# Performance work log

Measured on AMD Instinct MI355X. Metric: run time of the kernel, lower is better.

## Reference

```python
import jax, jax.numpy as jnp
import numpy as np

B, S, D = 2, 1024, 2048
H, KV, HD = 16, 4, 128
GROUPS = H // KV
THETA = 10000.0


def act_quant(xr, xi):
    # per-token 8-bit absmax quantization over last dim, joint scale for re/im, STE
    amax = jnp.maximum(jnp.max(jnp.abs(xr), -1, keepdims=True),
                       jnp.max(jnp.abs(xi), -1, keepdims=True))
    s = 127.0 / jnp.maximum(amax, 1e-5)
    qr = jnp.clip(jnp.round(xr * s), -128, 127) / s
    qi = jnp.clip(jnp.round(xi * s), -128, 127) / s
    return xr + jax.lax.stop_gradient(qr - xr), xi + jax.lax.stop_gradient(qi - xi)


def weight_quant(wr, wi):
    # Fairy+-i direction quantization: each weight -> scale * d, d in {+1,-1,+i,-i}; STE
    mag = jnp.mean(jnp.sqrt(wr * wr + wi * wi))
    use_re = jnp.abs(wr) >= jnp.abs(wi)
    qr = jnp.where(use_re, jnp.sign(wr) * mag, 0.0)
    qi = jnp.where(use_re, 0.0, jnp.sign(wi) * mag)
    return wr + jax.lax.stop_gradient(qr - wr), wi + jax.lax.stop_gradient(qi - wi)


def complex_linear(xr, xi, wr, wi):
    xr, xi = act_quant(xr, xi)
    wr, wi = weight_quant(wr, wi)
    o_re = xr @ wr - xi @ wi
    o_im = xr @ wi + xi @ wr
    return o_re, o_im


def rotate_half(x):
    h = x.shape[-1] // 2
    return jnp.concatenate([-x[..., h:], x[..., :h]], axis=-1)


def rope_tables():
    inv_freq = 1.0 / (THETA ** (jnp.arange(0, HD, 2, dtype=jnp.float32) / HD))
    pos = jnp.arange(S, dtype=jnp.float32)
    freqs = pos[:, None] * inv_freq[None, :]          # [S, HD/2]
    emb = jnp.concatenate([freqs, freqs], axis=-1)    # [S, HD]
    return jnp.cos(emb)[None, None], jnp.sin(emb)[None, None]  # [1,1,S,HD]


def _heads(x, n):
    # [B,S,n*HD] -> [B,n,S,HD]
    return x.reshape(B, S, n, HD).transpose(0, 2, 1, 3)


def _attn(hidden_real, hidden_imag, wq_re, wq_im, wk_re, wk_im,
          wv_re, wv_im, wo_re, wo_im):
    q_re, q_im = complex_linear(hidden_real, hidden_imag, wq_re, wq_im)
    k_re, k_im = complex_linear(hidden_real, hidden_imag, wk_re, wk_im)
    v_re, v_im = complex_linear(hidden_real, hidden_imag, wv_re, wv_im)

    q_re, q_im = _heads(q_re, H), _heads(q_im, H)      # [B,H,S,HD]
    k_re, k_im = _heads(k_re, KV), _heads(k_im, KV)    # [B,KV,S,HD]
    v_re, v_im = _heads(v_re, KV), _heads(v_im, KV)

    cos, sin = rope_tables()
    # RoPE applied only to real components of q and k
    q_re = q_re * cos + rotate_half(q_re) * sin
    k_re = k_re * cos + rotate_half(k_re) * sin

    # GQA repeat
    k_re = jnp.repeat(k_re, GROUPS, axis=1)
    k_im = jnp.repeat(k_im, GROUPS, axis=1)
    v_re = jnp.repeat(v_re, GROUPS, axis=1)
    v_im = jnp.repeat(v_im, GROUPS, axis=1)

    # real scores = Re(q . conj(k)) = q_re.k_re + q_im.k_im
    scores = (jnp.einsum('bhqd,bhkd->bhqk', q_re, k_re) +
              jnp.einsum('bhqd,bhkd->bhqk', q_im, k_im)) / jnp.sqrt(jnp.float32(HD))
    causal = jnp.tril(jnp.ones((S, S), dtype=bool))
    scores = jnp.where(causal[None, None], scores, jnp.finfo(scores.dtype).min)
    attn = jax.nn.softmax(scores, axis=-1)

    o_re = jnp.einsum('bhqk,bhkd->bhqd', attn, v_re)
    o_im = jnp.einsum('bhqk,bhkd->bhqd', attn, v_im)
    o_re = o_re.transpose(0, 2, 1, 3).reshape(B, S, H * HD)
    o_im = o_im.transpose(0, 2, 1, 3).reshape(B, S, H * HD)

    out_re, out_im = complex_linear(o_re, o_im, wo_re, wo_im)
    return jnp.stack([out_re, out_im])  # [2,B,S,D]


def setup_inputs() -> dict:
    key = jax.random.key(0)
    ks = jax.random.split(key, 12)
    w = lambda k, shp: jax.random.normal(k, shp, dtype=jnp.float32) * 0.02
    return {
        'hidden_real': jax.random.normal(ks[0], (B, S, D), dtype=jnp.float32),
        'hidden_imag': jax.random.normal(ks[1], (B, S, D), dtype=jnp.float32),
        'wq_re': w(ks[2], (D, H * HD)), 'wq_im': w(ks[3], (D, H * HD)),
        'wk_re': w(ks[4], (D, KV * HD)), 'wk_im': w(ks[5], (D, KV * HD)),
        'wv_re': w(ks[6], (D, KV * HD)), 'wv_im': w(ks[7], (D, KV * HD)),
        'wo_re': w(ks[8], (H * HD, D)), 'wo_im': w(ks[9], (H * HD, D)),
    }


def reference(hidden_real, hidden_imag, wq_re, wq_im, wk_re, wk_im,
              wv_re, wv_im, wo_re, wo_im):
    return _attn(hidden_real, hidden_imag, wq_re, wq_im, wk_re, wk_im,
                 wv_re, wv_im, wo_re, wo_im)
```

## Files before the change

### kernel.cpp

```cpp
#include <hip/hip_runtime.h>
#include <stdint.h>

#define B_   2
#define S_   1024
#define D_   2048
#define H_   16
#define KV_  4
#define HD_  128
#define NTOK (B_ * S_)
#define QD   (H_ * HD_)
#define KD   (KV_ * HD_)

using i32x4  = __attribute__((ext_vector_type(4)))  int;
using i32x16 = __attribute__((ext_vector_type(16))) int;
using f32x4  = __attribute__((ext_vector_type(4)))  float;
using bf16x8 = __attribute__((ext_vector_type(8)))  short;

#define LN1E4_OVER_64 0.14391156831212725f

__device__ __forceinline__ float bf2f(uint16_t u) { return __uint_as_float((uint32_t)u << 16); }
__device__ __forceinline__ uint16_t f2bf(float f) {
    uint32_t u = __float_as_uint(f);
    return (uint16_t)((u + 0x7FFFu + ((u >> 16) & 1u)) >> 16);
}

__device__ __forceinline__ i32x4 neg_i8x16(i32x4 x) {
    i32x4 r;
#pragma unroll
    for (int i = 0; i < 4; ++i) {
        uint32_t nx = ~(uint32_t)x[i];
        r[i] = (int)(((nx & 0x7F7F7F7Fu) + 0x01010101u) ^ (nx & 0x80808080u));
    }
    return r;
}

__global__ __launch_bounds__(256)
void act_quant_i8_kernel(const float* __restrict__ xr, const float* __restrict__ xi,
                         int8_t* __restrict__ qr, int8_t* __restrict__ qi,
                         float* __restrict__ invs)
{
    const int tok = blockIdx.x, t = threadIdx.x;
    const float* pr = xr + (size_t)tok * 2048 + t * 8;
    const float* pi = xi + (size_t)tok * 2048 + t * 8;
    float4 r0 = *(const float4*)pr, r1 = *(const float4*)(pr + 4);
    float4 i0 = *(const float4*)pi, i1 = *(const float4*)(pi + 4);
    float am = fmaxf(fmaxf(fmaxf(fabsf(r0.x), fabsf(r0.y)), fmaxf(fabsf(r0.z), fabsf(r0.w))),
                     fmaxf(fmaxf(fabsf(r1.x), fabsf(r1.y)), fmaxf(fabsf(r1.z), fabsf(r1.w))));
    am = fmaxf(am, fmaxf(fmaxf(fmaxf(fabsf(i0.x), fabsf(i0.y)), fmaxf(fabsf(i0.z), fabsf(i0.w))),
                         fmaxf(fmaxf(fabsf(i1.x), fabsf(i1.y)), fmaxf(fabsf(i1.z), fabsf(i1.w)))));
    __shared__ float red[256];
    red[t] = am;
    __syncthreads();
    for (int st = 128; st > 0; st >>= 1) {
        if (t < st) red[t] = fmaxf(red[t], red[t + st]);
        __syncthreads();
    }
    const float s = 127.0f / fmaxf(red[0], 1e-5f);
    if (t == 0) invs[tok] = 1.0f / s;
#define Q8(x) ((uint32_t)(uint8_t)(int8_t)(int)fminf(fmaxf(rintf((x) * s), -128.f), 127.f))
    uint32_t a0 = Q8(r0.x) | (Q8(r0.y) << 8) | (Q8(r0.z) << 16) | (Q8(r0.w) << 24);
    uint32_t a1 = Q8(r1.x) | (Q8(r1.y) << 8) | (Q8(r1.z) << 16) | (Q8(r1.w) << 24);
    uint32_t b0 = Q8(i0.x) | (Q8(i0.y) << 8) | (Q8(i0.z) << 16) | (Q8(i0.w) << 24);
    uint32_t b1 = Q8(i1.x) | (Q8(i1.y) << 8) | (Q8(i1.z) << 16) | (Q8(i1.w) << 24);
#undef Q8
    *(uint32_t*)(qr + (size_t)tok * 2048 + t * 8)     = a0;
    *(uint32_t*)(qr + (size_t)tok * 2048 + t * 8 + 4) = a1;
    *(uint32_t*)(qi + (size_t)tok * 2048 + t * 8)     = b0;
    *(uint32_t*)(qi + (size_t)tok * 2048 + t * 8 + 4) = b1;
}

__global__ __launch_bounds__(256)
void decode_kernel(const float* __restrict__ wr, const float* __restrict__ wi,
                   int N, int8_t* __restrict__ psr, int8_t* __restrict__ psi,
                   int n_off, float* __restrict__ mag_out)
{
    __shared__ alignas(16) int8_t tr[2][64][80];
    __shared__ float red[256];
    const int n0 = blockIdx.x * 64, k0 = blockIdx.y * 64;
    float msum = 0.f;
    for (int idx = threadIdx.x; idx < 4096; idx += 256) {
        int j = idx & 63, i = idx >> 6;
        size_t g = (size_t)(k0 + i) * N + n0 + j;
        float a = wr[g], b = wi[g];
        msum += sqrtf(a * a + b * b);
        int8_t sr, si;
        if (fabsf(a) >= fabsf(b)) {
            sr = (a > 0.f) ? 1 : ((a < 0.f) ? -1 : 0);
            si = 0;
        } else {
            sr = 0;
            si = (b > 0.f) ? 1 : ((b < 0.f) ? -1 : 0);
        }
        tr[0][j][i] = sr;
        tr[1][j][i] = si;
    }
    red[threadIdx.x] = msum;
    __syncthreads();
    for (int st = 128; st > 0; st >>= 1) {
        if (threadIdx.x < st) red[threadIdx.x] += red[threadIdx.x + st];
        __syncthreads();
    }
    if (threadIdx.x == 0) atomicAdd(mag_out, red[0]);
    int8_t* planes[2] = { psr, psi };
    for (int idx = threadIdx.x; idx < 512; idx += 256) {
        int p = idx >> 8, rem = idx & 255, n = rem >> 2, c = rem & 3;
        int4 v = *(const int4*)&tr[p][n][c * 16];
        *(int4*)(planes[p] + (size_t)(n_off + n0 + n) * 2048 + k0 + c * 16) = v;
    }
}

__device__ __forceinline__ void async_copy16(const void* g, void* l) {
    __builtin_amdgcn_global_load_lds((const __attribute__((address_space(1))) void*)g,
                                     (__attribute__((address_space(3))) void*)l, 16, 0, 0);
}

template <int MODE>
__global__ __launch_bounds__(256, 3)
void gemm_i8_kernel(const int8_t* __restrict__ axr, const int8_t* __restrict__ axi,
                    const int8_t* __restrict__ bsr, const int8_t* __restrict__ bsi,
                    int Nout, const float* __restrict__ invs,
                    const float* __restrict__ mag_sums,
                    float magc0, float magc1, float magc2,
                    float* o_re, float* o_im,
                    uint16_t* kbr, uint16_t* kbi, uint16_t* vbr, uint16_t* vbi)
{
    __shared__ alignas(16) int8_t smem[2][24576];
    const int tid = threadIdx.x;
    const int wav = tid >> 6, lane = tid & 63;
    const int tileM = blockIdx.y * 64, tileN = blockIdx.x * 128;
    const int K = 2048;

    i32x16 pre[2] = {};
    i32x16 pim[2] = {};

    auto issue_tile = [&](int k0, int buf) {
#pragma unroll
        for (int i = 0; i < 6; ++i) {
            int q = wav + 4 * i;
            const int8_t* g;
            int8_t* l;
            if (q < 8) {
                int pl = q >> 2, c = q & 3;
                g = (pl ? axi : axr) + (size_t)(tileM + lane) * K + k0 + c * 16;
                l = &smem[buf][pl * 4096 + (c * 64 + lane) * 16];
            } else {
                int r = q - 8;
                int pl = r >> 3, s = r & 7, c = s >> 1, m0 = (s & 1) << 6;
                g = (pl ? bsi : bsr) + (size_t)(tileN + m0 + lane) * K + k0 + c * 16;
                l = &smem[buf][8192 + pl * 8192 + (c * 128 + m0 + lane) * 16];
            }
            async_copy16(g, l);
        }
    };

    issue_tile(0, 0);
    issue_tile(64, 1);

    for (int k = 0; k < 32; ++k) {
        if (k == 31) { asm volatile("s_waitcnt vmcnt(0)" ::: "memory"); }
        else         { asm volatile("s_waitcnt vmcnt(6)" ::: "memory"); }
        asm volatile("s_barrier" ::: "memory");
        const int8_t* sb = smem[k & 1];
#pragma unroll
        for (int s = 0; s < 2; ++s) {
            const int cc = 2 * s + (lane >> 5);
            const int rA = lane & 31;
            const int rB = wav * 32 + (lane & 31);
            i32x4 fxr[2], fxi[2];
#pragma unroll
            for (int mb = 0; mb < 2; ++mb) {
                int off = (cc * 64 + rA + mb * 32) * 16;
                fxr[mb] = *(const i32x4*)&sb[off];
                fxi[mb] = *(const i32x4*)&sb[4096 + off];
            }
            i32x4 fbr, fbi;
            {
                int off = (cc * 128 + rB) * 16;
                fbr = *(const i32x4*)&sb[8192 + off];
                fbi = *(const i32x4*)&sb[16384 + off];
            }
            const i32x4 fbin = neg_i8x16(fbi);
#pragma unroll
            for (int mb = 0; mb < 2; ++mb) {
                pre[mb] = __builtin_amdgcn_mfma_i32_32x32x32_i8(fxr[mb], fbr,  pre[mb], 0, 0, 0);
                pre[mb] = __builtin_amdgcn_mfma_i32_32x32x32_i8(fxi[mb], fbin, pre[mb], 0, 0, 0);
                pim[mb] = __builtin_amdgcn_mfma_i32_32x32x32_i8(fxr[mb], fbi,  pim[mb], 0, 0, 0);
                pim[mb] = __builtin_amdgcn_mfma_i32_32x32x32_i8(fxi[mb], fbr,  pim[mb], 0, 0, 0);
            }
        }
        asm volatile("s_barrier" ::: "memory");
        if (k + 2 < 32) issue_tile((k + 2) * 64, k & 1);
    }

    const int ln31 = lane & 31, lq = lane >> 5;
    const int gn = tileN + wav * 32 + ln31;
    float mag;
    if (MODE == 0)
        mag = (gn < 2048) ? mag_sums[0] * magc0
            : (gn < 2560) ? mag_sums[1] * magc1
                          : mag_sums[2] * magc2;
    else
        mag = mag_sums[0] * magc0;
#pragma unroll
    for (int mb = 0; mb < 2; ++mb) {
#pragma unroll
        for (int r = 0; r < 16; ++r) {
            const int row = (r & 3) + 8 * (r >> 2) + 4 * lq;
            const int gm = tileM + mb * 32 + row;
            const float sc = mag * invs[gm];
            const float re = (float)pre[mb][r] * sc;
            const float im = (float)pim[mb][r] * sc;
            if (MODE == 1) {
                o_re[(size_t)gm * Nout + gn] = re;
                o_im[(size_t)gm * Nout + gn] = im;
            } else {
                const int s = gm & (S_ - 1), bb = gm >> 10;
                if (gn < 2048) {
                    o_re[(size_t)gm * 2048 + gn] = re;
                    o_im[(size_t)gm * 2048 + gn] = im;
                } else if (gn < 2560) {
                    int c = gn - 2048, kvh = c >> 7, d = c & 127;
                    size_t off = ((size_t)(bb * KV_ + kvh) * S_ + s) * 128 + d;
                    kbr[off] = f2bf(re);
                    kbi[off] = f2bf(im);
                } else {
                    int c = gn - 2560, kvh = c >> 7, d = c & 127;
                    size_t off = ((size_t)(bb * KV_ + kvh) * S_ + s) * 128 + d;
                    vbr[off] = f2bf(re);
                    vbi[off] = f2bf(im);
                }
            }
        }
    }
}

__global__ __launch_bounds__(256)
void rope_q_kernel(const float* __restrict__ q_re, const float* __restrict__ q_im,
                   uint16_t* __restrict__ qb_re, uint16_t* __restrict__ qb_im)
{
    int gidx = blockIdx.x * 256 + threadIdx.x;
    int j = gidx & 15, h = (gidx >> 4) & 15, tok = gidx >> 8;
    int s = tok & (S_ - 1), b = tok >> 10;
    int d0 = j * 4;
    size_t ib = (size_t)tok * 2048 + h * 128;
    float4 r0 = *(const float4*)&q_re[ib + d0];
    float4 r1 = *(const float4*)&q_re[ib + d0 + 64];
    float4 i0 = *(const float4*)&q_im[ib + d0];
    float4 i1 = *(const float4*)&q_im[ib + d0 + 64];
    float ro0[4], ro1[4];
    float rv0[4] = { r0.x, r0.y, r0.z, r0.w };
    float rv1[4] = { r1.x, r1.y, r1.z, r1.w };
#pragma unroll
    for (int t = 0; t < 4; ++t) {
        float f = __expf(-(float)(d0 + t) * LN1E4_OVER_64);
        float sn, c;
        __sincosf((float)s * f, &sn, &c);
        ro0[t] = rv0[t] * c - rv1[t] * sn;
        ro1[t] = rv1[t] * c + rv0[t] * sn;
    }
    size_t ob = ((size_t)(b * H_ + h) * S_ + s) * 128;
    ushort4 w;
    w = (ushort4){ f2bf(ro0[0]), f2bf(ro0[1]), f2bf(ro0[2]), f2bf(ro0[3]) };
    *(ushort4*)&qb_re[ob + d0] = w;
    w = (ushort4){ f2bf(ro1[0]), f2bf(ro1[1]), f2bf(ro1[2]), f2bf(ro1[3]) };
    *(ushort4*)&qb_re[ob + d0 + 64] = w;
    w = (ushort4){ f2bf(i0.x), f2bf(i0.y), f2bf(i0.z), f2bf(i0.w) };
    *(ushort4*)&qb_im[ob + d0] = w;
    w = (ushort4){ f2bf(i1.x), f2bf(i1.y), f2bf(i1.z), f2bf(i1.w) };
    *(ushort4*)&qb_im[ob + d0 + 64] = w;
}

__global__ __launch_bounds__(256)
void rope_k_kernel(uint16_t* __restrict__ kb_re)
{
    int gidx = blockIdx.x * 256 + threadIdx.x;
    int j = gidx & 15, kvh = (gidx >> 4) & 3;
    int rest = gidx >> 6;
    int s = rest & (S_ - 1), b = rest >> 10;
    int d0 = j * 4;
    size_t base = ((size_t)(b * KV_ + kvh) * S_ + s) * 128;
    ushort4 u0 = *(const ushort4*)&kb_re[base + d0];
    ushort4 u1 = *(const ushort4*)&kb_re[base + d0 + 64];
    float rv0[4] = { bf2f(u0.x), bf2f(u0.y), bf2f(u0.z), bf2f(u0.w) };
    float rv1[4] = { bf2f(u1.x), bf2f(u1.y), bf2f(u1.z), bf2f(u1.w) };
    float ro0[4], ro1[4];
#pragma unroll
    for (int t = 0; t < 4; ++t) {
        float f = __expf(-(float)(d0 + t) * LN1E4_OVER_64);
        float sn, c;
        __sincosf((float)s * f, &sn, &c);
        ro0[t] = rv0[t] * c - rv1[t] * sn;
        ro1[t] = rv1[t] * c + rv0[t] * sn;
    }
    *(ushort4*)&kb_re[base + d0]      = (ushort4){ f2bf(ro0[0]), f2bf(ro0[1]), f2bf(ro0[2]), f2bf(ro0[3]) };
    *(ushort4*)&kb_re[base + d0 + 64] = (ushort4){ f2bf(ro1[0]), f2bf(ro1[1]), f2bf(ro1[2]), f2bf(ro1[3]) };
}

__global__ __launch_bounds__(256)
void vtrans_kernel(const uint16_t* __restrict__ vbr, const uint16_t* __restrict__ vbi,
                   uint16_t* __restrict__ vtr, uint16_t* __restrict__ vti)
{
    __shared__ uint16_t t[32][36];
    const int pl = blockIdx.z & 1, bk = blockIdx.z >> 1;
    const int s0 = blockIdx.x * 32, d0 = blockIdx.y * 32;
    const uint16_t* src = (pl ? vbi : vbr) + ((size_t)bk * S_) * 128;
    uint16_t*       dst = (pl ? vti : vtr) + ((size_t)bk * 128) * S_;
    const int r = threadIdx.x >> 3, c = (threadIdx.x & 7) * 4;
    *(ushort4*)&t[r][c] = *(const ushort4*)&src[(size_t)(s0 + r) * 128 + d0 + c];
    __syncthreads();
    ushort4 o = (ushort4){ t[c][r], t[c + 1][r], t[c + 2][r], t[c + 3][r] };
    *(ushort4*)&dst[(size_t)(d0 + r) * S_ + s0 + c] = o;
}

__global__ __launch_bounds__(256)
void attn_mfma_kernel(const uint16_t* __restrict__ qb_re, const uint16_t* __restrict__ qb_im,
                      const uint16_t* __restrict__ kb_re, const uint16_t* __restrict__ kb_im,
                      const uint16_t* __restrict__ vt_re, const uint16_t* __restrict__ vt_im,
                      float* __restrict__ o_re, float* __restrict__ o_im)
{
    __shared__ alignas(16) uint16_t sbuf[2][16384];
    __shared__ alignas(16) uint16_t sp[4][16][40];

    const int tid = threadIdx.x;
    const int w = tid >> 6, lane = tid & 63;
    const int r16 = lane & 15, q4 = lane >> 4;
    const int h = blockIdx.y, b = blockIdx.z;
    const int qt = b ? blockIdx.x : (gridDim.x - 1 - blockIdx.x);
    const int kvh = h >> 2;
    const int q0 = qt * 64, qw0 = q0 + w * 16;

    bf16x8 qfr[4], qfi[4];
    {
        const size_t qbase = ((size_t)(b * H_ + h) * S_ + qw0 + r16) * 128;
#pragma unroll
        for (int ks = 0; ks < 4; ++ks) {
            const int col = ks * 32 + q4 * 8;
            qfr[ks] = *(const bf16x8*)&qb_re[qbase + col];
            qfi[ks] = *(const bf16x8*)&qb_im[qbase + col];
        }
    }

    f32x4 oa[2][8] = {};
    float m_r[4] = { -3e38f, -3e38f, -3e38f, -3e38f };
    float l_r[4] = { 0.f, 0.f, 0.f, 0.f };

    const size_t kgbase0 = (size_t)(b * KV_ + kvh) * S_ * 128;
    const uint16_t* vre = vt_re + (size_t)(b * KV_ + kvh) * 128 * (size_t)S_;
    const uint16_t* vim = vt_im + (size_t)(b * KV_ + kvh) * 128 * (size_t)S_;

    const uint16_t* kp[4];
    const uint16_t* vp[4];
#pragma unroll
    for (int i = 0; i < 4; ++i) {
        const int kch = (i & 1) * 8 + w * 2 + (lane >> 5);
        kp[i] = ((i >> 1) ? kb_im : kb_re) + kgbase0 + (size_t)(lane & 31) * 128 + kch * 8;
        const int vch = (i & 1) * 2 + (w >> 1);
        const int vd  = ((w & 1) << 6) | lane;
        vp[i] = ((i >> 1) ? vim : vre) + (size_t)vd * S_ + vch * 8;
    }

    auto issue_tile = [&](int kt, int buf) {
#pragma unroll
        for (int i = 0; i < 4; ++i)
            async_copy16(kp[i] + (size_t)kt * 4096, &sbuf[buf][w * 512 + i * 2048]);
#pragma unroll
        for (int i = 0; i < 4; ++i)
            async_copy16(vp[i] + (size_t)kt * 32, &sbuf[buf][8192 + w * 512 + i * 2048]);
    };

    const int nk = (q0 + 64) >> 5;

    issue_tile(0, 0);
    issue_tile(1, 1);

    for (int k = 0; k < nk; ++k) {
        if (k == nk - 1) { asm volatile("s_waitcnt vmcnt(0)" ::: "memory"); }
        else             { asm volatile("s_waitcnt vmcnt(8)" ::: "memory"); }
        asm volatile("s_barrier" ::: "memory");
        const uint16_t* sb = sbuf[k & 1];
        const int c0 = k << 5;

        if (c0 <= qw0 + 15) {
            f32x4 sc[2] = {};
#pragma unroll
            for (int cblk = 0; cblk < 2; ++cblk) {
                const int krow = cblk * 16 + r16;
#pragma unroll
                for (int ks = 0; ks < 4; ++ks) {
                    const int koff = (ks * 4 + q4) * 256 + krow * 8;
                    bf16x8 kr = *(const bf16x8*)&sb[koff];
                    bf16x8 ki = *(const bf16x8*)&sb[4096 + koff];
                    sc[cblk] = __builtin_amdgcn_mfma_f32_16x16x32_bf16(qfr[ks], kr, sc[cblk], 0, 0, 0);
                    sc[cblk] = __builtin_amdgcn_mfma_f32_16x16x32_bf16(qfi[ks], ki, sc[cblk], 0, 0, 0);
                }
            }
#pragma unroll
            for (int cblk = 0; cblk < 2; ++cblk)
#pragma unroll
                for (int reg = 0; reg < 4; ++reg) {
                    float sval = sc[cblk][reg] * 0.08838834764831845f;
                    const int rowg = qw0 + q4 * 4 + reg;
                    const int colg = c0 + cblk * 16 + r16;
                    if (colg > rowg) sval = -3e38f;
                    sc[cblk][reg] = sval;
                }
            float al[4];
#pragma unroll
            for (int reg = 0; reg < 4; ++reg) {
                float mx = fmaxf(sc[0][reg], sc[1][reg]);
#pragma unroll
                for (int msk = 1; msk < 16; msk <<= 1) mx = fmaxf(mx, __shfl_xor(mx, msk));
                const float mn = fmaxf(m_r[reg], mx);
                al[reg] = __expf(m_r[reg] - mn);
                const float p0 = __expf(sc[0][reg] - mn);
                const float p1 = __expf(sc[1][reg] - mn);
                sc[0][reg] = p0; sc[1][reg] = p1;
                float rs = p0 + p1;
#pragma unroll
                for (int msk = 1; msk < 16; msk <<= 1) rs += __shfl_xor(rs, msk);
                l_r[reg] = l_r[reg] * al[reg] + rs;
                m_r[reg] = mn;
            }
#pragma unroll
            for (int cblk = 0; cblk < 2; ++cblk)
#pragma unroll
                for (int reg = 0; reg < 4; ++reg)
                    sp[w][q4 * 4 + reg][cblk * 16 + r16] = f2bf(sc[cblk][reg]);
#pragma unroll
            for (int dblk = 0; dblk < 8; ++dblk)
#pragma unroll
                for (int reg = 0; reg < 4; ++reg) {
                    oa[0][dblk][reg] *= al[reg];
                    oa[1][dblk][reg] *= al[reg];
                }
            bf16x8 pf = *(const bf16x8*)&sp[w][r16][q4 * 8];
#pragma unroll
            for (int dblk = 0; dblk < 8; ++dblk) {
                const int voff = 8192 + q4 * 1024 + (dblk * 16 + r16) * 8;
                bf16x8 vr = *(const bf16x8*)&sb[voff];
                bf16x8 vi = *(const bf16x8*)&sb[4096 + voff];
                oa[0][dblk] = __builtin_amdgcn_mfma_f32_16x16x32_bf16(pf, vr, oa[0][dblk], 0, 0, 0);
                oa[1][dblk] = __builtin_amdgcn_mfma_f32_16x16x32_bf16(pf, vi, oa[1][dblk], 0, 0, 0);
            }
        }

        asm volatile("s_barrier" ::: "memory");
        if (k + 2 < nk) issue_tile(k + 2, k & 1);
    }

    float inv[4];
#pragma unroll
    for (int reg = 0; reg < 4; ++reg) inv[reg] = 1.f / l_r[reg];
#pragma unroll
    for (int dblk = 0; dblk < 8; ++dblk) {
        const int col = h * 128 + dblk * 16 + r16;
#pragma unroll
        for (int reg = 0; reg < 4; ++reg) {
            const size_t tok = (size_t)b * S_ + qw0 + q4 * 4 + reg;
            o_re[tok * 2048 + col] = oa[0][dblk][reg] * inv[reg];
            o_im[tok * 2048 + col] = oa[1][dblk][reg] * inv[reg];
        }
    }
}

extern "C" void kernel_launch(void* const* d_in, const int* in_sizes, int n_in,
                              void* d_out, int out_size, void* d_ws, size_t ws_size,
                              hipStream_t stream)
{
    const float* hr    = (const float*)d_in[0];
    const float* hi    = (const float*)d_in[1];
    const float* wq_re = (const float*)d_in[2];
    const float* wq_im = (const float*)d_in[3];
    const float* wk_re = (const float*)d_in[4];
    const float* wk_im = (const float*)d_in[5];
    const float* wv_re = (const float*)d_in[6];
    const float* wv_im = (const float*)d_in[7];
    const float* wo_re = (const float*)d_in[8];
    const float* wo_im = (const float*)d_in[9];
    float* out = (float*)d_out;
    char*  base = (char*)d_ws;

    const size_t MB4  = (size_t)2048 * 2048;
    const size_t QKVP = (size_t)3072 * 2048;
    const size_t KVE  = (size_t)B_ * KV_ * S_ * 128;

    float*   mags   = (float*)(base);
    float*   invs1  = (float*)(base + 1024);
    float*   invs2  = (float*)(base + 9216);
    int8_t*  xr_q   = (int8_t*)(base + 32768);
    int8_t*  xi_q   = xr_q + MB4;
    int8_t*  qkv_sr = xi_q + MB4;
    int8_t*  qkv_si = qkv_sr + QKVP;
    int8_t*  qkv_ns = qkv_si + QKVP;
    int8_t*  wo_sr  = qkv_ns + QKVP;
    int8_t*  wo_si  = wo_sr + MB4;
    int8_t*  wo_ns  = wo_si + MB4;
    float*   q_re   = (float*)(wo_ns + MB4);
    float*   q_im   = q_re + MB4;
    uint16_t* kb_re = (uint16_t*)(q_im + MB4);
    uint16_t* kb_im = kb_re + KVE;
    uint16_t* vb_re = kb_im + KVE;
    uint16_t* vb_im = vb_re + KVE;
    uint16_t* vt_re = (uint16_t*)xr_q;
    uint16_t* vt_im = (uint16_t*)xi_q;
    uint16_t* qb_re = (uint16_t*)qkv_sr;
    uint16_t* qb_im = (uint16_t*)(qkv_sr + 8388608);

    hipMemsetAsync(mags, 0, 16, stream);

    decode_kernel<<<dim3(32, 32), 256, 0, stream>>>(wq_re, wq_im, 2048, qkv_sr, qkv_si, 0,    mags + 0);
    decode_kernel<<<dim3(8, 32),  256, 0, stream>>>(wk_re, wk_im, 512,  qkv_sr, qkv_si, 2048, mags + 1);
    decode_kernel<<<dim3(8, 32),  256, 0, stream>>>(wv_re, wv_im, 512,  qkv_sr, qkv_si, 2560, mags + 2);
    decode_kernel<<<dim3(32, 32), 256, 0, stream>>>(wo_re, wo_im, 2048, wo_sr, wo_si, 0,      mags + 3);

    act_quant_i8_kernel<<<NTOK, 256, 0, stream>>>(hr, hi, xr_q, xi_q, invs1);

    gemm_i8_kernel<0><<<dim3(24, 32), 256, 0, stream>>>(
        xr_q, xi_q, qkv_sr, qkv_si, 0, invs1, mags,
        1.0f / (float)((size_t)D_ * QD), 1.0f / (float)((size_t)D_ * KD), 1.0f / (float)((size_t)D_ * KD),
        q_re, q_im, kb_re, kb_im, vb_re, vb_im);

    rope_q_kernel<<<NTOK * H_ * 16 / 256, 256, 0, stream>>>(q_re, q_im, qb_re, qb_im);
    rope_k_kernel<<<NTOK * KV_ * 16 / 256, 256, 0, stream>>>(kb_re);
    vtrans_kernel<<<dim3(S_ / 32, 128 / 32, B_ * KV_ * 2), 256, 0, stream>>>(vb_re, vb_im, vt_re, vt_im);

    attn_mfma_kernel<<<dim3(S_ / 64, H_, B_), 256, 0, stream>>>(
        qb_re, qb_im, kb_re, kb_im, vt_re, vt_im, q_re, q_im);

    act_quant_i8_kernel<<<NTOK, 256, 0, stream>>>(q_re, q_im, xr_q, xi_q, invs2);

    gemm_i8_kernel<1><<<dim3(16, 32), 256, 0, stream>>>(
        xr_q, xi_q, wo_sr, wo_si, 2048, invs2, mags + 3,
        1.0f / (float)((size_t)QD * D_), 0.f, 0.f,
        out, out + MB4, nullptr, nullptr, nullptr, nullptr);
}
```

Before: 464.2 us.

## Fuse RoPE into QKV GEMM epilogue and emit bf16 attention output

The QKV GEMM epilogue now applies RoPE directly, using an LDS exchange to fetch the rotate-half partner column, and writes bf16 Q and K in head-major layout. This removes the separate rope_q and rope_k kernels and the fp32 Q round trip through global memory. The attention kernel now writes bf16 output, and a new bf16-input activation quantizer reads it, halving that traffic. The cost is an extra LDS pass and barriers in the GEMM epilogue, plus bf16 rounding of the attention output before quantization, which could slightly change the quantized values.

```diff
diff --git a/kernel.cpp b/kernel.cpp
--- a/kernel.cpp
+++ b/kernel.cpp
@@ -62,6 +62,48 @@
     uint32_t a1 = Q8(r1.x) | (Q8(r1.y) << 8) | (Q8(r1.z) << 16) | (Q8(r1.w) << 24);
     uint32_t b0 = Q8(i0.x) | (Q8(i0.y) << 8) | (Q8(i0.z) << 16) | (Q8(i0.w) << 24);
     uint32_t b1 = Q8(i1.x) | (Q8(i1.y) << 8) | (Q8(i1.z) << 16) | (Q8(i1.w) << 24);
+#undef Q8
+    *(uint32_t*)(qr + (size_t)tok * 2048 + t * 8)     = a0;
+    *(uint32_t*)(qr + (size_t)tok * 2048 + t * 8 + 4) = a1;
+    *(uint32_t*)(qi + (size_t)tok * 2048 + t * 8)     = b0;
+    *(uint32_t*)(qi + (size_t)tok * 2048 + t * 8 + 4) = b1;
+}
+
+__global__ __launch_bounds__(256)
+void act_quant_bf16_kernel(const uint16_t* __restrict__ xr, const uint16_t* __restrict__ xi,
+                           int8_t* __restrict__ qr, int8_t* __restrict__ qi,
+                           float* __restrict__ invs)
+{
+    const int tok = blockIdx.x, t = threadIdx.x;
+    uint4 rv = *(const uint4*)(xr + (size_t)tok * 2048 + t * 8);
+    uint4 iv = *(const uint4*)(xi + (size_t)tok * 2048 + t * 8);
+    float fr[8], fi[8];
+    const uint32_t* ru = (const uint32_t*)&rv;
+    const uint32_t* iu = (const uint32_t*)&iv;
+#pragma unroll
+    for (int i = 0; i < 4; ++i) {
+        fr[2 * i]     = __uint_as_float(ru[i] << 16);
+        fr[2 * i + 1] = __uint_as_float(ru[i] & 0xFFFF0000u);
+        fi[2 * i]     = __uint_as_float(iu[i] << 16);
+        fi[2 * i + 1] = __uint_as_float(iu[i] & 0xFFFF0000u);
+    }
+    float am = 0.f;
+#pragma unroll
+    for (int i = 0; i < 8; ++i) am = fmaxf(am, fmaxf(fabsf(fr[i]), fabsf(fi[i])));
+    __shared__ float red[256];
+    red[t] = am;
+    __syncthreads();
+    for (int st = 128; st > 0; st >>= 1) {
+        if (t < st) red[t] = fmaxf(red[t], red[t + st]);
+        __syncthreads();
+    }
+    const float s = 127.0f / fmaxf(red[0], 1e-5f);
+    if (t == 0) invs[tok] = 1.0f / s;
+#define Q8(x) ((uint32_t)(uint8_t)(int8_t)(int)fminf(fmaxf(rintf((x) * s), -128.f), 127.f))
+    uint32_t a0 = Q8(fr[0]) | (Q8(fr[1]) << 8) | (Q8(fr[2]) << 16) | (Q8(fr[3]) << 24);
+    uint32_t a1 = Q8(fr[4]) | (Q8(fr[5]) << 8) | (Q8(fr[6]) << 16) | (Q8(fr[7]) << 24);
+    uint32_t b0 = Q8(fi[0]) | (Q8(fi[1]) << 8) | (Q8(fi[2]) << 16) | (Q8(fi[3]) << 24);
+    uint32_t b1 = Q8(fi[4]) | (Q8(fi[5]) << 8) | (Q8(fi[6]) << 16) | (Q8(fi[7]) << 24);
 #undef Q8
     *(uint32_t*)(qr + (size_t)tok * 2048 + t * 8)     = a0;
     *(uint32_t*)(qr + (size_t)tok * 2048 + t * 8 + 4) = a1;
@@ -122,6 +164,7 @@
                     const float* __restrict__ mag_sums,
                     float magc0, float magc1, float magc2,
                     float* o_re, float* o_im,
+                    uint16_t* qbr, uint16_t* qbi,
                     uint16_t* kbr, uint16_t* kbi, uint16_t* vbr, uint16_t* vbi)
 {
     __shared__ alignas(16) int8_t smem[2][24576];
@@ -201,99 +244,68 @@
                           : mag_sums[2] * magc2;
     else
         mag = mag_sums[0] * magc0;
-#pragma unroll
-    for (int mb = 0; mb < 2; ++mb) {
-#pragma unroll
-        for (int r = 0; r < 16; ++r) {
-            const int row = (r & 3) + 8 * (r >> 2) + 4 * lq;
-            const int gm = tileM + mb * 32 + row;
-            const float sc = mag * invs[gm];
-            const float re = (float)pre[mb][r] * sc;
-            const float im = (float)pim[mb][r] * sc;
-            if (MODE == 1) {
-                o_re[(size_t)gm * Nout + gn] = re;
-                o_im[(size_t)gm * Nout + gn] = im;
-            } else {
+
+    if (MODE == 0 && tileN < 2560) {
+        float* lds_ex = (float*)smem;
+        const int d = wav * 32 + ln31;
+        __syncthreads();
+#pragma unroll
+        for (int mb = 0; mb < 2; ++mb)
+#pragma unroll
+            for (int r = 0; r < 16; ++r) {
+                const int row = mb * 32 + (r & 3) + 8 * (r >> 2) + 4 * lq;
+                lds_ex[d * 65 + row] = (float)pre[mb][r] * (mag * invs[tileM + row]);
+            }
+        __syncthreads();
+        const float fd = __expf(-(float)(d & 63) * LN1E4_OVER_64);
+#pragma unroll
+        for (int mb = 0; mb < 2; ++mb)
+#pragma unroll
+            for (int r = 0; r < 16; ++r) {
+                const int row = mb * 32 + (r & 3) + 8 * (r >> 2) + 4 * lq;
+                const int gm = tileM + row;
                 const int s = gm & (S_ - 1), bb = gm >> 10;
-                if (gn < 2048) {
-                    o_re[(size_t)gm * 2048 + gn] = re;
-                    o_im[(size_t)gm * 2048 + gn] = im;
-                } else if (gn < 2560) {
-                    int c = gn - 2048, kvh = c >> 7, d = c & 127;
-                    size_t off = ((size_t)(bb * KV_ + kvh) * S_ + s) * 128 + d;
-                    kbr[off] = f2bf(re);
+                const float sc = mag * invs[gm];
+                const float re = (float)pre[mb][r] * sc;
+                const float im = (float)pim[mb][r] * sc;
+                const float prt = lds_ex[(d ^ 64) * 65 + row];
+                float sn, cs;
+                __sincosf((float)s * fd, &sn, &cs);
+                const float ro = (d < 64) ? (re * cs - prt * sn) : (re * cs + prt * sn);
+                if (tileN < 2048) {
+                    const int hh = tileN >> 7;
+                    const size_t off = ((size_t)(bb * H_ + hh) * S_ + s) * 128 + d;
+                    qbr[off] = f2bf(ro);
+                    qbi[off] = f2bf(im);
+                } else {
+                    const int kvh = (tileN - 2048) >> 7;
+                    const size_t off = ((size_t)(bb * KV_ + kvh) * S_ + s) * 128 + d;
+                    kbr[off] = f2bf(ro);
                     kbi[off] = f2bf(im);
+                }
+            }
+    } else {
+#pragma unroll
+        for (int mb = 0; mb < 2; ++mb)
+#pragma unroll
+            for (int r = 0; r < 16; ++r) {
+                const int row = (r & 3) + 8 * (r >> 2) + 4 * lq;
+                const int gm = tileM + mb * 32 + row;
+                const float sc = mag * invs[gm];
+                const float re = (float)pre[mb][r] * sc;
+                const float im = (float)pim[mb][r] * sc;
+                if (MODE == 1) {
+                    o_re[(size_t)gm * Nout + gn] = re;
+                    o_im[(size_t)gm * Nout + gn] = im;
                 } else {
-                    int c = gn - 2560, kvh = c >> 7, d = c & 127;
-                    size_t off = ((size_t)(bb * KV_ + kvh) * S_ + s) * 128 + d;
+                    const int s = gm & (S_ - 1), bb = gm >> 10;
+                    const int c = gn - 2560, kvh = c >> 7, dd = c & 127;
+                    const size_t off = ((size_t)(bb * KV_ + kvh) * S_ + s) * 128 + dd;
                     vbr[off] = f2bf(re);
                     vbi[off] = f2bf(im);
                 }
             }
-        }
-    }
-}
-
-__global__ __launch_bounds__(256)
-void rope_q_kernel(const float* __restrict__ q_re, const float* __restrict__ q_im,
-                   uint16_t* __restrict__ qb_re, uint16_t* __restrict__ qb_im)
-{
-    int gidx = blockIdx.x * 256 + threadIdx.x;
-    int j = gidx & 15, h = (gidx >> 4) & 15, tok = gidx >> 8;
-    int s = tok & (S_ - 1), b = tok >> 10;
-    int d0 = j * 4;
-    size_t ib = (size_t)tok * 2048 + h * 128;
-    float4 r0 = *(const float4*)&q_re[ib + d0];
-    float4 r1 = *(const float4*)&q_re[ib + d0 + 64];
-    float4 i0 = *(const float4*)&q_im[ib + d0];
-    float4 i1 = *(const float4*)&q_im[ib + d0 + 64];
-    float ro0[4], ro1[4];
-    float rv0[4] = { r0.x, r0.y, r0.z, r0.w };
-    float rv1[4] = { r1.x, r1.y, r1.z, r1.w };
-#pragma unroll
-    for (int t = 0; t < 4; ++t) {
-        float f = __expf(-(float)(d0 + t) * LN1E4_OVER_64);
-        float sn, c;
-        __sincosf((float)s * f, &sn, &c);
-        ro0[t] = rv0[t] * c - rv1[t] * sn;
-        ro1[t] = rv1[t] * c + rv0[t] * sn;
-    }
-    size_t ob = ((size_t)(b * H_ + h) * S_ + s) * 128;
-    ushort4 w;
-    w = (ushort4){ f2bf(ro0[0]), f2bf(ro0[1]), f2bf(ro0[2]), f2bf(ro0[3]) };
-    *(ushort4*)&qb_re[ob + d0] = w;
-    w = (ushort4){ f2bf(ro1[0]), f2bf(ro1[1]), f2bf(ro1[2]), f2bf(ro1[3]) };
-    *(ushort4*)&qb_re[ob + d0 + 64] = w;
-    w = (ushort4){ f2bf(i0.x), f2bf(i0.y), f2bf(i0.z), f2bf(i0.w) };
-    *(ushort4*)&qb_im[ob + d0] = w;
-    w = (ushort4){ f2bf(i1.x), f2bf(i1.y), f2bf(i1.z), f2bf(i1.w) };
-    *(ushort4*)&qb_im[ob + d0 + 64] = w;
-}
-
-__global__ __launch_bounds__(256)
-void rope_k_kernel(uint16_t* __restrict__ kb_re)
-{
-    int gidx = blockIdx.x * 256 + threadIdx.x;
-    int j = gidx & 15, kvh = (gidx >> 4) & 3;
-    int rest = gidx >> 6;
-    int s = rest & (S_ - 1), b = rest >> 10;
-    int d0 = j * 4;
-    size_t base = ((size_t)(b * KV_ + kvh) * S_ + s) * 128;
-    ushort4 u0 = *(const ushort4*)&kb_re[base + d0];
-    ushort4 u1 = *(const ushort4*)&kb_re[base + d0 + 64];
-    float rv0[4] = { bf2f(u0.x), bf2f(u0.y), bf2f(u0.z), bf2f(u0.w) };
-    float rv1[4] = { bf2f(u1.x), bf2f(u1.y), bf2f(u1.z), bf2f(u1.w) };
-    float ro0[4], ro1[4];
-#pragma unroll
-    for (int t = 0; t < 4; ++t) {
-        float f = __expf(-(float)(d0 + t) * LN1E4_OVER_64);
-        float sn, c;
-        __sincosf((float)s * f, &sn, &c);
-        ro0[t] = rv0[t] * c - rv1[t] * sn;
-        ro1[t] = rv1[t] * c + rv0[t] * sn;
-    }
-    *(ushort4*)&kb_re[base + d0]      = (ushort4){ f2bf(ro0[0]), f2bf(ro0[1]), f2bf(ro0[2]), f2bf(ro0[3]) };
-    *(ushort4*)&kb_re[base + d0 + 64] = (ushort4){ f2bf(ro1[0]), f2bf(ro1[1]), f2bf(ro1[2]), f2bf(ro1[3]) };
+    }
 }
 
 __global__ __launch_bounds__(256)
@@ -316,7 +328,7 @@
 void attn_mfma_kernel(const uint16_t* __restrict__ qb_re, const uint16_t* __restrict__ qb_im,
                       const uint16_t* __restrict__ kb_re, const uint16_t* __restrict__ kb_im,
                       const uint16_t* __restrict__ vt_re, const uint16_t* __restrict__ vt_im,
-                      float* __restrict__ o_re, float* __restrict__ o_im)
+                      uint16_t* __restrict__ ob_re, uint16_t* __restrict__ ob_im)
 {
     __shared__ alignas(16) uint16_t sbuf[2][16384];
     __shared__ alignas(16) uint16_t sp[4][16][40];
@@ -457,8 +469,8 @@
 #pragma unroll
         for (int reg = 0; reg < 4; ++reg) {
             const size_t tok = (size_t)b * S_ + qw0 + q4 * 4 + reg;
-            o_re[tok * 2048 + col] = oa[0][dblk][reg] * inv[reg];
-            o_im[tok * 2048 + col] = oa[1][dblk][reg] * inv[reg];
+            ob_re[tok * 2048 + col] = f2bf(oa[0][dblk][reg] * inv[reg]);
+            ob_im[tok * 2048 + col] = f2bf(oa[1][dblk][reg] * inv[reg]);
         }
     }
 }
@@ -503,8 +515,10 @@
     uint16_t* vb_im = vb_re + KVE;
     uint16_t* vt_re = (uint16_t*)xr_q;
     uint16_t* vt_im = (uint16_t*)xi_q;
-    uint16_t* qb_re = (uint16_t*)qkv_sr;
-    uint16_t* qb_im = (uint16_t*)(qkv_sr + 8388608);
+    uint16_t* qb_re = (uint16_t*)q_re;
+    uint16_t* qb_im = (uint16_t*)q_im;
+    uint16_t* ob_re = (uint16_t*)qkv_sr;
+    uint16_t* ob_im = (uint16_t*)(qkv_sr + 8388608);
 
     hipMemsetAsync(mags, 0, 16, stream);
 
@@ -518,19 +532,17 @@
     gemm_i8_kernel<0><<<dim3(24, 32), 256, 0, stream>>>(
         xr_q, xi_q, qkv_sr, qkv_si, 0, invs1, mags,
         1.0f / (float)((size_t)D_ * QD), 1.0f / (float)((size_t)D_ * KD), 1.0f / (float)((size_t)D_ * KD),
-        q_re, q_im, kb_re, kb_im, vb_re, vb_im);
-
-    rope_q_kernel<<<NTOK * H_ * 16 / 256, 256, 0, stream>>>(q_re, q_im, qb_re, qb_im);
-    rope_k_kernel<<<NTOK * KV_ * 16 / 256, 256, 0, stream>>>(kb_re);
+        nullptr, nullptr, qb_re, qb_im, kb_re, kb_im, vb_re, vb_im);
+
     vtrans_kernel<<<dim3(S_ / 32, 128 / 32, B_ * KV_ * 2), 256, 0, stream>>>(vb_re, vb_im, vt_re, vt_im);
 
     attn_mfma_kernel<<<dim3(S_ / 64, H_, B_), 256, 0, stream>>>(
-        qb_re, qb_im, kb_re, kb_im, vt_re, vt_im, q_re, q_im);
-
-    act_quant_i8_kernel<<<NTOK, 256, 0, stream>>>(q_re, q_im, xr_q, xi_q, invs2);
+        qb_re, qb_im, kb_re, kb_im, vt_re, vt_im, ob_re, ob_im);
+
+    act_quant_bf16_kernel<<<NTOK, 256, 0, stream>>>(ob_re, ob_im, xr_q, xi_q, invs2);
 
     gemm_i8_kernel<1><<<dim3(16, 32), 256, 0, stream>>>(
         xr_q, xi_q, wo_sr, wo_si, 2048, invs2, mags + 3,
         1.0f / (float)((size_t)QD * D_), 0.f, 0.f,
-        out, out + MB4, nullptr, nullptr, nullptr, nullptr);
-}
+        out, out + MB4, nullptr, nullptr, nullptr, nullptr, nullptr, nullptr);
+}
```

Result: faster. 449.2 us (-3.2%).
